# Optimization experiments

Hardware: AMD Instinct MI355X
Metric: run time of the kernel (lower is better)

The kernel has to match this reference:

```python
import jax, jax.numpy as jnp
import numpy as np

C_IN, C_OUT, KH, KW = 64, 128, 3, 3
STRIDE, PAD, DIL = 1, 1, 1
EPS = 1e-5


def setup_inputs() -> dict:
    key = jax.random.key(0)
    ks = jax.random.split(key, 7)
    B, H, W = 8, 112, 112
    x = jax.random.normal(ks[0], (B, C_IN, H, W), dtype=jnp.float32)
    # offset conv: produces 2*KH*KW offset channels; small init keeps offsets sane
    w_off = jax.random.normal(ks[1], (2 * KH * KW, C_IN, KH, KW), dtype=jnp.float32) * 0.01
    b_off = jax.random.normal(ks[2], (2 * KH * KW,), dtype=jnp.float32) * 0.01
    # deformable conv weight/bias
    fan_in = C_IN * KH * KW
    w_dcn = jax.random.normal(ks[3], (C_OUT, C_IN, KH, KW), dtype=jnp.float32) / np.sqrt(fan_in)
    b_dcn = jax.random.normal(ks[4], (C_OUT,), dtype=jnp.float32) * 0.01
    gamma = jnp.ones((C_OUT,), dtype=jnp.float32)
    beta = jnp.zeros((C_OUT,), dtype=jnp.float32)
    return {"x": x, "w_off": w_off, "b_off": b_off, "w_dcn": w_dcn,
            "b_dcn": b_dcn, "gamma": gamma, "beta": beta}


def _conv2d(x, w, b):
    y = jax.lax.conv_general_dilated(
        x, w, window_strides=(STRIDE, STRIDE),
        padding=((PAD, PAD), (PAD, PAD)),
        rhs_dilation=(DIL, DIL),
        dimension_numbers=("NCHW", "OIHW", "NCHW"))
    return y + b[None, :, None, None]


def _deform_conv(x, offset, w, b):
    # x: [B,C,H,W]; offset: [B, 2*KH*KW, Ho, Wo] with (dy, dx) pairs per tap
    B, C, H, W = x.shape
    KK = KH * KW
    Ho, Wo = offset.shape[2], offset.shape[3]
    off = offset.reshape(B, KK, 2, Ho, Wo)
    ky = (jnp.arange(KK) // KW).astype(jnp.float32)  # kernel row per tap
    kx = (jnp.arange(KK) % KW).astype(jnp.float32)
    base_y = (jnp.arange(Ho) * STRIDE - PAD).astype(jnp.float32)
    base_x = (jnp.arange(Wo) * STRIDE - PAD).astype(jnp.float32)
    # sampling positions [B, KK, Ho, Wo]
    py = off[:, :, 0] + base_y[None, None, :, None] + (ky * DIL)[None, :, None, None]
    px = off[:, :, 1] + base_x[None, None, None, :] + (kx * DIL)[None, :, None, None]

    y0 = jnp.floor(py)
    x0 = jnp.floor(px)
    wy1 = py - y0  # weight for y0+1
    wx1 = px - x0
    y0i = y0.astype(jnp.int32)
    x0i = x0.astype(jnp.int32)

    x_flat = x.reshape(B, C, H * W)

    def gather_corner(yi, xi, wgt):
        # yi, xi, wgt: [B, KK, Ho, Wo]
        valid = (yi >= 0) & (yi < H) & (xi >= 0) & (xi < W)
        idx = jnp.clip(yi, 0, H - 1) * W + jnp.clip(xi, 0, W - 1)
        idx = idx.reshape(B, -1)  # [B, KK*Ho*Wo]
        vals = jnp.take_along_axis(x_flat, idx[:, None, :], axis=2)  # [B, C, N]
        coef = (wgt * valid.astype(wgt.dtype)).reshape(B, 1, -1)
        return vals * coef

    samp = (gather_corner(y0i,     x0i,     (1 - wy1) * (1 - wx1))
            + gather_corner(y0i,     x0i + 1, (1 - wy1) * wx1)
            + gather_corner(y0i + 1, x0i,     wy1 * (1 - wx1))
            + gather_corner(y0i + 1, x0i + 1, wy1 * wx1))
    samp = samp.reshape(B, C, KK, Ho, Wo)
    out = jnp.einsum("bckhw,ock->bohw", samp, w.reshape(w.shape[0], C, KK))
    return out + b[None, :, None, None]


def reference(x, w_off, b_off, w_dcn, b_dcn, gamma, beta):
    offset = _conv2d(x, w_off, b_off)
    y = _deform_conv(x, offset, w_dcn, b_dcn)
    # BatchNorm2d (training mode: biased batch stats) + ReLU
    mean = jnp.mean(y, axis=(0, 2, 3))
    var = jnp.var(y, axis=(0, 2, 3))
    yhat = (y - mean[None, :, None, None]) * jax.lax.rsqrt(var + EPS)[None, :, None, None]
    y = gamma[None, :, None, None] * yhat + beta[None, :, None, None]
    return jax.nn.relu(y)
```

## Files before the change

kernel.cpp:

```cpp
#include <hip/hip_runtime.h>

#define H    112
#define W    112
#define HW   12544
#define CIN  64
#define COUT 128
#define BATCH 8
#define KK   9
#define OFFC 18
#define EPS  1e-5f
#define TP   32
#define KDIM 576
#define KHALF 288
#define KPAD2 296
#define NB   3136
#define YPAD 36

typedef unsigned short ushort;
typedef unsigned int uint;
typedef _Float16 half2v __attribute__((ext_vector_type(2)));
typedef _Float16 half8  __attribute__((ext_vector_type(8)));
typedef __attribute__((ext_vector_type(4))) float floatx4;

__device__ __forceinline__ half2v u2h(uint u) {
  union { uint u; half2v h; } c; c.u = u; return c.h;
}
__device__ __forceinline__ uint h2u(half2v h) {
  union { uint u; half2v h; } c; c.h = h; return c.u;
}
__device__ __forceinline__ uint pack_h2(float a, float b) {
  half2v h; h[0] = (_Float16)a; h[1] = (_Float16)b; return h2u(h);
}
__device__ __forceinline__ ushort f2h_bits(float v) {
  union { _Float16 h; ushort u; } c; c.h = (_Float16)v; return c.u;
}
__device__ __forceinline__ float h2f_bits(ushort u) {
  union { ushort u; _Float16 h; } c; c.u = u; return (float)c.h;
}

__global__ __launch_bounds__(256) void k_transpose_x(
    const float* __restrict__ x, ushort* __restrict__ xTh) {
  __shared__ float tile[64][65];
  int b = blockIdx.y;
  int p0 = blockIdx.x * 64;
  int tid = threadIdx.x;
  int j = tid & 63, cb = tid >> 6;
#pragma unroll
  for (int i = 0; i < 16; ++i) {
    int ci = cb * 16 + i;
    tile[ci][j] = x[((size_t)(b * CIN + ci)) * HW + p0 + j];
  }
  __syncthreads();
  int px = tid >> 2, ciq = tid & 3;
#pragma unroll
  for (int g = 0; g < 4; ++g) {
    int ci = ciq * 16 + g * 4;
    uint lo = pack_h2(tile[ci + 0][px], tile[ci + 1][px]);
    uint hi = pack_h2(tile[ci + 2][px], tile[ci + 3][px]);
    *(uint2*)&xTh[((size_t)b * HW + p0 + px) * 64 + ci] = make_uint2(lo, hi);
  }
}

__global__ __launch_bounds__(256) void k_prep_w(
    const float* __restrict__ w_off, const float* __restrict__ w_dcn,
    ushort* __restrict__ w_offT, ushort* __restrict__ w_mf) {
  int i = blockIdx.x * 256 + threadIdx.x;
  if (i < 32 * KDIM) {
    int oc = i / KDIM, k = i - oc * KDIM;
    int kk = k >> 6, ci = k & 63;
    float v = (oc < OFFC) ? w_off[(oc * CIN + ci) * KK + kk] : 0.f;
    w_offT[i] = f2h_bits(v);
  } else if (i < 32 * KDIM + COUT * KDIM) {
    int jj = i - 32 * KDIM;
    int co = jj / KDIM, k = jj - co * KDIM;
    int h = k / KHALF, r = k - h * KHALF;
    int kk = r >> 5, cil = r & 31;
    int ci = h * 32 + cil;
    w_mf[jj] = f2h_bits(w_dcn[(co * CIN + ci) * KK + kk]);
  }
}

__global__ __launch_bounds__(256) void k_offset_conv(
    const ushort* __restrict__ xTh, const ushort* __restrict__ w_offT,
    const float* __restrict__ bias, float* __restrict__ out) {
  int b = blockIdx.y;
  int wave = threadIdx.x >> 6, lane = threadIdx.x & 63;
  int row16 = lane & 15, quad = lane >> 4;
  int p = blockIdx.x * 64 + wave * 16 + row16;
  int ho = p / W, wo = p - ho * W;
  const ushort* xb = xTh + (size_t)b * HW * 64;

  half8 Bf[18];
#pragma unroll
  for (int ks = 0; ks < 18; ++ks) {
    int kk = ks >> 1;
    int ci0 = (ks & 1) * 32 + quad * 8;
    int kh = kk / 3, kw = kk - kh * 3;
    int yy = ho + kh - 1, xx = wo + kw - 1;
    bool valid = (yy >= 0) & (yy < H) & (xx >= 0) & (xx < W);
    half8 v = {0, 0, 0, 0, 0, 0, 0, 0};
    if (valid) v = *(const half8*)(xb + ((size_t)(yy * W + xx) << 6) + ci0);
    Bf[ks] = v;
  }
  floatx4 acc0 = {0.f, 0.f, 0.f, 0.f}, acc1 = acc0;
  const ushort* wa0 = w_offT + row16 * KDIM + quad * 8;
  const ushort* wa1 = w_offT + (16 + row16) * KDIM + quad * 8;
#pragma unroll
  for (int ks = 0; ks < 18; ++ks) {
    half8 A0 = *(const half8*)(wa0 + ks * 32);
    half8 A1 = *(const half8*)(wa1 + ks * 32);
    acc0 = __builtin_amdgcn_mfma_f32_16x16x32_f16(A0, Bf[ks], acc0, 0, 0, 0);
    acc1 = __builtin_amdgcn_mfma_f32_16x16x32_f16(A1, Bf[ks], acc1, 0, 0, 0);
  }
  float* ob = out + (size_t)b * OFFC * HW;
#pragma unroll
  for (int reg = 0; reg < 4; ++reg) {
    int oc = quad * 4 + reg;
    ob[(size_t)oc * HW + p] = acc0[reg] + bias[oc];
    int oc1 = 16 + oc;
    if (oc1 < OFFC) ob[(size_t)oc1 * HW + p] = acc1[reg] + bias[oc1];
  }
}

struct SMemA { uint4 s_wh[KK][TP]; int4 s_i[KK][TP]; ushort samp[TP][KPAD2]; };
struct SMemB { ushort yst[COUT][YPAD]; float stat_s[COUT]; float stat_q[COUT]; };
union SMemU { SMemA a; SMemB b; };

__global__ __launch_bounds__(256) void k_deform(
    const ushort* __restrict__ xTh, const float* __restrict__ off,
    const ushort* __restrict__ w_mf, ushort* __restrict__ y,
    float* __restrict__ psT) {
  __shared__ SMemU sm;

  int b = blockIdx.y;
  int p0 = blockIdx.x * TP;
  int bid = blockIdx.y * gridDim.x + blockIdx.x;
  int tid = threadIdx.x;
  const ushort* xb = xTh + (size_t)b * HW * 64;

  for (int it = tid; it < KK * TP; it += 256) {
    int kk = it >> 5;
    int px = it & 31;
    int p = p0 + px;
    int ho = p / W, wo = p - ho * W;
    float dy = off[((size_t)b * OFFC + 2 * kk) * HW + p];
    float dx = off[((size_t)b * OFFC + 2 * kk + 1) * HW + p];
    float py = dy + (float)(ho - 1 + kk / 3);
    float pxx = dx + (float)(wo - 1 + kk % 3);
    float y0f = floorf(py), x0f = floorf(pxx);
    float wy1 = py - y0f, wx1 = pxx - x0f;
    int y0 = (int)y0f, x0 = (int)x0f;
    int y1 = y0 + 1, x1 = x0 + 1;
    float vy0 = (y0 >= 0 && y0 < H) ? 1.f : 0.f;
    float vy1 = (y1 >= 0 && y1 < H) ? 1.f : 0.f;
    float vx0 = (x0 >= 0 && x0 < W) ? 1.f : 0.f;
    float vx1 = (x1 >= 0 && x1 < W) ? 1.f : 0.f;
    int cy0 = min(max(y0, 0), H - 1), cy1 = min(max(y1, 0), H - 1);
    int cx0 = min(max(x0, 0), W - 1), cx1 = min(max(x1, 0), W - 1);
    float w00 = (1.f - wy1) * (1.f - wx1) * vy0 * vx0;
    float w01 = (1.f - wy1) * wx1 * vy0 * vx1;
    float w10 = wy1 * (1.f - wx1) * vy1 * vx0;
    float w11 = wy1 * wx1 * vy1 * vx1;
    sm.a.s_wh[kk][px] = make_uint4(pack_h2(w00, w00), pack_h2(w01, w01),
                                   pack_h2(w10, w10), pack_h2(w11, w11));
    sm.a.s_i[kk][px] = make_int4((cy0 * W + cx0) << 6, (cy0 * W + cx1) << 6,
                                 (cy1 * W + cx0) << 6, (cy1 * W + cx1) << 6);
  }
  __syncthreads();

  int wave = tid >> 6, lane = tid & 63;
  int row16 = lane & 15, quad = lane >> 4;
  int koff = quad * 8;
  int co_base = wave * 32;
  const ushort* wa0 = w_mf + (size_t)(co_base + row16) * KDIM + koff;
  const ushort* wa1 = w_mf + (size_t)(co_base + 16 + row16) * KDIM + koff;

  floatx4 acc00 = {0.f, 0.f, 0.f, 0.f}, acc01 = acc00, acc10 = acc00, acc11 = acc00;

  for (int h = 0; h < 2; ++h) {
#pragma unroll
    for (int r = 0; r < 5; ++r) {
      int it = tid + r * 256;
      if (it < 1152) {
        int px = it / 36;
        int rem = it - px * 36;
        int kk = rem >> 2;
        int cig = rem & 3;
        int cil0 = cig * 8;
        int cio = h * 32 + cil0;
        uint4 wh = sm.a.s_wh[kk][px];
        int4 iv = sm.a.s_i[kk][px];
        half2v w0 = u2h(wh.x), w1 = u2h(wh.y), w2 = u2h(wh.z), w3 = u2h(wh.w);
        uint4 c0 = *(const uint4*)(xb + iv.x + cio);
        uint4 c1 = *(const uint4*)(xb + iv.y + cio);
        uint4 c2 = *(const uint4*)(xb + iv.z + cio);
        uint4 c3 = *(const uint4*)(xb + iv.w + cio);
        uint4 res;
        res.x = h2u(w0 * u2h(c0.x) + w1 * u2h(c1.x) + w2 * u2h(c2.x) + w3 * u2h(c3.x));
        res.y = h2u(w0 * u2h(c0.y) + w1 * u2h(c1.y) + w2 * u2h(c2.y) + w3 * u2h(c3.y));
        res.z = h2u(w0 * u2h(c0.z) + w1 * u2h(c1.z) + w2 * u2h(c2.z) + w3 * u2h(c3.z));
        res.w = h2u(w0 * u2h(c0.w) + w1 * u2h(c1.w) + w2 * u2h(c2.w) + w3 * u2h(c3.w));
        *(uint4*)&sm.a.samp[px][kk * 32 + cil0] = res;
      }
    }
    __syncthreads();

    const ushort* sb0 = &sm.a.samp[row16][koff];
    const ushort* sb1 = &sm.a.samp[16 + row16][koff];
    const ushort* a0 = wa0 + h * KHALF;
    const ushort* a1 = wa1 + h * KHALF;
#pragma unroll
    for (int ks = 0; ks < 9; ++ks) {
      half8 A0 = *(const half8*)(a0 + ks * 32);
      half8 A1 = *(const half8*)(a1 + ks * 32);
      half8 B0 = *(const half8*)(sb0 + ks * 32);
      half8 B1 = *(const half8*)(sb1 + ks * 32);
      acc00 = __builtin_amdgcn_mfma_f32_16x16x32_f16(A0, B0, acc00, 0, 0, 0);
      acc01 = __builtin_amdgcn_mfma_f32_16x16x32_f16(A0, B1, acc01, 0, 0, 0);
      acc10 = __builtin_amdgcn_mfma_f32_16x16x32_f16(A1, B0, acc10, 0, 0, 0);
      acc11 = __builtin_amdgcn_mfma_f32_16x16x32_f16(A1, B1, acc11, 0, 0, 0);
    }
    __syncthreads();
  }

#pragma unroll
  for (int reg = 0; reg < 4; ++reg) {
    int cA = co_base + quad * 4 + reg;
    int cB = cA + 16;
    sm.b.yst[cA][row16]      = f2h_bits(acc00[reg]);
    sm.b.yst[cA][16 + row16] = f2h_bits(acc01[reg]);
    sm.b.yst[cB][row16]      = f2h_bits(acc10[reg]);
    sm.b.yst[cB][16 + row16] = f2h_bits(acc11[reg]);
    float s0 = acc00[reg] + acc01[reg];
    float q0 = acc00[reg] * acc00[reg] + acc01[reg] * acc01[reg];
    float s1 = acc10[reg] + acc11[reg];
    float q1 = acc10[reg] * acc10[reg] + acc11[reg] * acc11[reg];
#pragma unroll
    for (int m = 1; m < 16; m <<= 1) {
      s0 += __shfl_xor(s0, m, 64);
      q0 += __shfl_xor(q0, m, 64);
      s1 += __shfl_xor(s1, m, 64);
      q1 += __shfl_xor(q1, m, 64);
    }
    if (row16 == 0) {
      sm.b.stat_s[cA] = s0;
      sm.b.stat_q[cA] = q0;
      sm.b.stat_s[cB] = s1;
      sm.b.stat_q[cB] = q1;
    }
  }
  __syncthreads();

  {
    int co = tid >> 1, seg = tid & 1;
    const ushort* row = &sm.b.yst[co][seg * 16];
    uint2 v0 = *(const uint2*)(row + 0);
    uint2 v1 = *(const uint2*)(row + 4);
    uint2 v2 = *(const uint2*)(row + 8);
    uint2 v3 = *(const uint2*)(row + 12);
    ushort* dst = y + (size_t)b * COUT * HW + (size_t)co * HW + p0 + seg * 16;
    *(uint4*)dst       = make_uint4(v0.x, v0.y, v1.x, v1.y);
    *(uint4*)(dst + 8) = make_uint4(v2.x, v2.y, v3.x, v3.y);
    float sv = (tid < 128) ? sm.b.stat_s[tid] : sm.b.stat_q[tid - 128];
    psT[(size_t)bid * 256 + tid] = sv;
  }
}

__global__ __launch_bounds__(256) void k_reduce(const float* __restrict__ psT,
                                                float* __restrict__ stats) {
  int tid = threadIdx.x;
  float s = 0.f;
  for (int i = blockIdx.x; i < NB; i += gridDim.x)
    s += psT[(size_t)i * 256 + tid];
  atomicAdd(&stats[tid], s);
}

__global__ __launch_bounds__(256) void k_norm(const ushort* __restrict__ y,
                                              const float* __restrict__ stats,
                                              const float* __restrict__ gamma,
                                              const float* __restrict__ beta,
                                              float* __restrict__ out) {
  int i8 = blockIdx.x * 256 + threadIdx.x;
  const int total8 = BATCH * COUT * HW / 8;
  if (i8 >= total8) return;
  size_t i = (size_t)i8 * 8;
  int c = (int)((i / HW) & (COUT - 1));
  const float N = (float)(BATCH * HW);
  float m = stats[c] / N;
  float var = stats[COUT + c] / N - m * m;
  float r = rsqrtf(var + EPS);
  float g = gamma[c], bt = beta[c];
  float a = r * g;
  float base = bt - m * a;
  uint4 u = *(const uint4*)&y[i];
  float4 o0, o1;
  half2v h0 = u2h(u.x), h1 = u2h(u.y), h2 = u2h(u.z), h3 = u2h(u.w);
  o0.x = fmaxf(0.f, fmaf((float)h0[0], a, base));
  o0.y = fmaxf(0.f, fmaf((float)h0[1], a, base));
  o0.z = fmaxf(0.f, fmaf((float)h1[0], a, base));
  o0.w = fmaxf(0.f, fmaf((float)h1[1], a, base));
  o1.x = fmaxf(0.f, fmaf((float)h2[0], a, base));
  o1.y = fmaxf(0.f, fmaf((float)h2[1], a, base));
  o1.z = fmaxf(0.f, fmaf((float)h3[0], a, base));
  o1.w = fmaxf(0.f, fmaf((float)h3[1], a, base));
  *(float4*)&out[i]     = o0;
  *(float4*)&out[i + 4] = o1;
}

extern "C" void kernel_launch(void* const* d_in, const int* in_sizes, int n_in,
                              void* d_out, int out_size, void* d_ws, size_t ws_size,
                              hipStream_t stream) {
  const float* x     = (const float*)d_in[0];
  const float* w_off = (const float*)d_in[1];
  const float* b_off = (const float*)d_in[2];
  const float* w_dcn = (const float*)d_in[3];
  const float* gamma = (const float*)d_in[5];
  const float* beta  = (const float*)d_in[6];
  float* out = (float*)d_out;

  float* ws = (float*)d_ws;
  float*  off_buf = ws;
  float*  psT     = off_buf + 1806336;
  float*  stats   = psT + 802816;
  ushort* xTh     = (ushort*)(stats + 256);
  ushort* w_mf    = xTh + 6422528;
  ushort* w_offT  = w_mf + 73728;
  ushort* y_h     = w_offT + 18432;

  hipMemsetAsync(stats, 0, 256 * sizeof(float), stream);
  k_transpose_x<<<dim3(HW / 64, BATCH), 256, 0, stream>>>(x, xTh);
  k_prep_w<<<(32 * KDIM + COUT * KDIM + 255) / 256, 256, 0, stream>>>(w_off, w_dcn, w_offT, w_mf);
  k_offset_conv<<<dim3(HW / 64, BATCH), 256, 0, stream>>>(xTh, w_offT, b_off, off_buf);
  k_deform<<<dim3(HW / TP, BATCH), 256, 0, stream>>>(xTh, off_buf, w_mf, y_h, psT);
  k_reduce<<<64, 256, 0, stream>>>(psT, stats);
  k_norm<<<(BATCH * COUT * HW / 8 + 255) / 256, 256, 0, stream>>>(y_h, stats, gamma, beta, out);
}
```

Measured before the change: 243.0 us.

## Fuse offset conv into deform kernel, merge prep kernels, rewrite stats reduction

The offset convolution is now computed inside the deformable kernel per 32-pixel tile with MFMA and kept in shared memory, which removes the global offset buffer round trip and one launch. The x transpose and weight prep kernels are merged into one launch. The stats reduction now has each block own four channels and reduce over all partial blocks with shuffles, which drops the memset and the atomics. The cost is extra register pressure and latency at the start of the deform kernel.

```diff
diff --git a/kernel.cpp b/kernel.cpp
--- a/kernel.cpp
+++ b/kernel.cpp
@@ -34,91 +34,47 @@
 __device__ __forceinline__ ushort f2h_bits(float v) {
   union { _Float16 h; ushort u; } c; c.h = (_Float16)v; return c.u;
 }
-__device__ __forceinline__ float h2f_bits(ushort u) {
-  union { ushort u; _Float16 h; } c; c.u = u; return (float)c.h;
-}
-
-__global__ __launch_bounds__(256) void k_transpose_x(
-    const float* __restrict__ x, ushort* __restrict__ xTh) {
+
+__global__ __launch_bounds__(256) void k_transpose_prep(
+    const float* __restrict__ x, const float* __restrict__ w_off,
+    const float* __restrict__ w_dcn, ushort* __restrict__ xTh,
+    ushort* __restrict__ w_offT, ushort* __restrict__ w_mf) {
   __shared__ float tile[64][65];
-  int b = blockIdx.y;
-  int p0 = blockIdx.x * 64;
+  int tb = blockIdx.x;
   int tid = threadIdx.x;
-  int j = tid & 63, cb = tid >> 6;
-#pragma unroll
-  for (int i = 0; i < 16; ++i) {
-    int ci = cb * 16 + i;
-    tile[ci][j] = x[((size_t)(b * CIN + ci)) * HW + p0 + j];
-  }
-  __syncthreads();
-  int px = tid >> 2, ciq = tid & 3;
-#pragma unroll
-  for (int g = 0; g < 4; ++g) {
-    int ci = ciq * 16 + g * 4;
-    uint lo = pack_h2(tile[ci + 0][px], tile[ci + 1][px]);
-    uint hi = pack_h2(tile[ci + 2][px], tile[ci + 3][px]);
-    *(uint2*)&xTh[((size_t)b * HW + p0 + px) * 64 + ci] = make_uint2(lo, hi);
-  }
-}
-
-__global__ __launch_bounds__(256) void k_prep_w(
-    const float* __restrict__ w_off, const float* __restrict__ w_dcn,
-    ushort* __restrict__ w_offT, ushort* __restrict__ w_mf) {
-  int i = blockIdx.x * 256 + threadIdx.x;
-  if (i < 32 * KDIM) {
-    int oc = i / KDIM, k = i - oc * KDIM;
-    int kk = k >> 6, ci = k & 63;
-    float v = (oc < OFFC) ? w_off[(oc * CIN + ci) * KK + kk] : 0.f;
-    w_offT[i] = f2h_bits(v);
-  } else if (i < 32 * KDIM + COUT * KDIM) {
-    int jj = i - 32 * KDIM;
-    int co = jj / KDIM, k = jj - co * KDIM;
-    int h = k / KHALF, r = k - h * KHALF;
-    int kk = r >> 5, cil = r & 31;
-    int ci = h * 32 + cil;
-    w_mf[jj] = f2h_bits(w_dcn[(co * CIN + ci) * KK + kk]);
-  }
-}
-
-__global__ __launch_bounds__(256) void k_offset_conv(
-    const ushort* __restrict__ xTh, const ushort* __restrict__ w_offT,
-    const float* __restrict__ bias, float* __restrict__ out) {
-  int b = blockIdx.y;
-  int wave = threadIdx.x >> 6, lane = threadIdx.x & 63;
-  int row16 = lane & 15, quad = lane >> 4;
-  int p = blockIdx.x * 64 + wave * 16 + row16;
-  int ho = p / W, wo = p - ho * W;
-  const ushort* xb = xTh + (size_t)b * HW * 64;
-
-  half8 Bf[18];
-#pragma unroll
-  for (int ks = 0; ks < 18; ++ks) {
-    int kk = ks >> 1;
-    int ci0 = (ks & 1) * 32 + quad * 8;
-    int kh = kk / 3, kw = kk - kh * 3;
-    int yy = ho + kh - 1, xx = wo + kw - 1;
-    bool valid = (yy >= 0) & (yy < H) & (xx >= 0) & (xx < W);
-    half8 v = {0, 0, 0, 0, 0, 0, 0, 0};
-    if (valid) v = *(const half8*)(xb + ((size_t)(yy * W + xx) << 6) + ci0);
-    Bf[ks] = v;
-  }
-  floatx4 acc0 = {0.f, 0.f, 0.f, 0.f}, acc1 = acc0;
-  const ushort* wa0 = w_offT + row16 * KDIM + quad * 8;
-  const ushort* wa1 = w_offT + (16 + row16) * KDIM + quad * 8;
-#pragma unroll
-  for (int ks = 0; ks < 18; ++ks) {
-    half8 A0 = *(const half8*)(wa0 + ks * 32);
-    half8 A1 = *(const half8*)(wa1 + ks * 32);
-    acc0 = __builtin_amdgcn_mfma_f32_16x16x32_f16(A0, Bf[ks], acc0, 0, 0, 0);
-    acc1 = __builtin_amdgcn_mfma_f32_16x16x32_f16(A1, Bf[ks], acc1, 0, 0, 0);
-  }
-  float* ob = out + (size_t)b * OFFC * HW;
-#pragma unroll
-  for (int reg = 0; reg < 4; ++reg) {
-    int oc = quad * 4 + reg;
-    ob[(size_t)oc * HW + p] = acc0[reg] + bias[oc];
-    int oc1 = 16 + oc;
-    if (oc1 < OFFC) ob[(size_t)oc1 * HW + p] = acc1[reg] + bias[oc1];
+  if (tb < 1568) {
+    int b = tb / 196;
+    int p0 = (tb - b * 196) * 64;
+    int j = tid & 63, cb = tid >> 6;
+#pragma unroll
+    for (int i = 0; i < 16; ++i) {
+      int ci = cb * 16 + i;
+      tile[ci][j] = x[((size_t)(b * CIN + ci)) * HW + p0 + j];
+    }
+    __syncthreads();
+    int px = tid >> 2, ciq = tid & 3;
+#pragma unroll
+    for (int g = 0; g < 4; ++g) {
+      int ci = ciq * 16 + g * 4;
+      uint lo = pack_h2(tile[ci + 0][px], tile[ci + 1][px]);
+      uint hi = pack_h2(tile[ci + 2][px], tile[ci + 3][px]);
+      *(uint2*)&xTh[((size_t)b * HW + p0 + px) * 64 + ci] = make_uint2(lo, hi);
+    }
+  } else {
+    int i = (tb - 1568) * 256 + tid;
+    if (i < 32 * KDIM) {
+      int oc = i / KDIM, k = i - oc * KDIM;
+      int kk = k >> 6, ci = k & 63;
+      float v = (oc < OFFC) ? w_off[(oc * CIN + ci) * KK + kk] : 0.f;
+      w_offT[i] = f2h_bits(v);
+    } else if (i < 32 * KDIM + COUT * KDIM) {
+      int jj = i - 32 * KDIM;
+      int co = jj / KDIM, k = jj - co * KDIM;
+      int h = k / KHALF, r = k - h * KHALF;
+      int kk = r >> 5, cil = r & 31;
+      int ci = h * 32 + cil;
+      w_mf[jj] = f2h_bits(w_dcn[(co * CIN + ci) * KK + kk]);
+    }
   }
 }
 
@@ -127,10 +83,11 @@
 union SMemU { SMemA a; SMemB b; };
 
 __global__ __launch_bounds__(256) void k_deform(
-    const ushort* __restrict__ xTh, const float* __restrict__ off,
-    const ushort* __restrict__ w_mf, ushort* __restrict__ y,
-    float* __restrict__ psT) {
+    const ushort* __restrict__ xTh, const ushort* __restrict__ w_offT,
+    const float* __restrict__ b_off, const ushort* __restrict__ w_mf,
+    ushort* __restrict__ y, float* __restrict__ psT) {
   __shared__ SMemU sm;
+  __shared__ float off_s[OFFC][33];
 
   int b = blockIdx.y;
   int p0 = blockIdx.x * TP;
@@ -138,13 +95,53 @@
   int tid = threadIdx.x;
   const ushort* xb = xTh + (size_t)b * HW * 64;
 
+  int wave = tid >> 6, lane = tid & 63;
+  int row16 = lane & 15, quad = lane >> 4;
+
+  {
+    int pxh = wave >> 1, mt = wave & 1;
+    int p = p0 + pxh * 16 + row16;
+    int ho = p / W, wo = p - ho * W;
+    floatx4 oacc = {0.f, 0.f, 0.f, 0.f};
+    const ushort* wa = w_offT + (size_t)(mt * 16 + row16) * KDIM + quad * 8;
+    half8 Bf[9];
+#pragma unroll
+    for (int c = 0; c < 2; ++c) {
+#pragma unroll
+      for (int j = 0; j < 9; ++j) {
+        int ks = c * 9 + j;
+        int kk = ks >> 1;
+        int ci0 = (ks & 1) * 32 + quad * 8;
+        int kh = kk / 3, kw = kk - kh * 3;
+        int yy = ho + kh - 1, xx = wo + kw - 1;
+        bool valid = (yy >= 0) & (yy < H) & (xx >= 0) & (xx < W);
+        half8 v = {0, 0, 0, 0, 0, 0, 0, 0};
+        if (valid) v = *(const half8*)(xb + ((size_t)(yy * W + xx) << 6) + ci0);
+        Bf[j] = v;
+      }
+#pragma unroll
+      for (int j = 0; j < 9; ++j) {
+        int ks = c * 9 + j;
+        half8 A = *(const half8*)(wa + ks * 32);
+        oacc = __builtin_amdgcn_mfma_f32_16x16x32_f16(A, Bf[j], oacc, 0, 0, 0);
+      }
+    }
+#pragma unroll
+    for (int reg = 0; reg < 4; ++reg) {
+      int oc = mt * 16 + quad * 4 + reg;
+      if (oc < OFFC)
+        off_s[oc][pxh * 16 + row16] = oacc[reg] + b_off[oc];
+    }
+  }
+  __syncthreads();
+
   for (int it = tid; it < KK * TP; it += 256) {
     int kk = it >> 5;
     int px = it & 31;
     int p = p0 + px;
     int ho = p / W, wo = p - ho * W;
-    float dy = off[((size_t)b * OFFC + 2 * kk) * HW + p];
-    float dx = off[((size_t)b * OFFC + 2 * kk + 1) * HW + p];
+    float dy = off_s[2 * kk][px];
+    float dx = off_s[2 * kk + 1][px];
     float py = dy + (float)(ho - 1 + kk / 3);
     float pxx = dx + (float)(wo - 1 + kk % 3);
     float y0f = floorf(py), x0f = floorf(pxx);
@@ -168,8 +165,6 @@
   }
   __syncthreads();
 
-  int wave = tid >> 6, lane = tid & 63;
-  int row16 = lane & 15, quad = lane >> 4;
   int koff = quad * 8;
   int co_base = wave * 32;
   const ushort* wa0 = w_mf + (size_t)(co_base + row16) * KDIM + koff;
@@ -268,11 +263,32 @@
 
 __global__ __launch_bounds__(256) void k_reduce(const float* __restrict__ psT,
                                                 float* __restrict__ stats) {
+  int g = blockIdx.x;
   int tid = threadIdx.x;
-  float s = 0.f;
-  for (int i = blockIdx.x; i < NB; i += gridDim.x)
-    s += psT[(size_t)i * 256 + tid];
-  atomicAdd(&stats[tid], s);
+  float4 a = make_float4(0.f, 0.f, 0.f, 0.f);
+  for (int i = tid; i < NB; i += 256) {
+    float4 v = *(const float4*)&psT[(size_t)i * 256 + g * 4];
+    a.x += v.x; a.y += v.y; a.z += v.z; a.w += v.w;
+  }
+#pragma unroll
+  for (int o = 32; o > 0; o >>= 1) {
+    a.x += __shfl_down(a.x, o, 64);
+    a.y += __shfl_down(a.y, o, 64);
+    a.z += __shfl_down(a.z, o, 64);
+    a.w += __shfl_down(a.w, o, 64);
+  }
+  __shared__ float4 ls[4];
+  int lane = tid & 63, wid = tid >> 6;
+  if (lane == 0) ls[wid] = a;
+  __syncthreads();
+  if (tid == 0) {
+    float4 s;
+    s.x = ls[0].x + ls[1].x + ls[2].x + ls[3].x;
+    s.y = ls[0].y + ls[1].y + ls[2].y + ls[3].y;
+    s.z = ls[0].z + ls[1].z + ls[2].z + ls[3].z;
+    s.w = ls[0].w + ls[1].w + ls[2].w + ls[3].w;
+    *(float4*)&stats[g * 4] = s;
+  }
 }
 
 __global__ __launch_bounds__(256) void k_norm(const ushort* __restrict__ y,
@@ -319,19 +335,15 @@
   float* out = (float*)d_out;
 
   float* ws = (float*)d_ws;
-  float*  off_buf = ws;
-  float*  psT     = off_buf + 1806336;
+  float*  psT     = ws;
   float*  stats   = psT + 802816;
   ushort* xTh     = (ushort*)(stats + 256);
   ushort* w_mf    = xTh + 6422528;
   ushort* w_offT  = w_mf + 73728;
   ushort* y_h     = w_offT + 18432;
 
-  hipMemsetAsync(stats, 0, 256 * sizeof(float), stream);
-  k_transpose_x<<<dim3(HW / 64, BATCH), 256, 0, stream>>>(x, xTh);
-  k_prep_w<<<(32 * KDIM + COUT * KDIM + 255) / 256, 256, 0, stream>>>(w_off, w_dcn, w_offT, w_mf);
-  k_offset_conv<<<dim3(HW / 64, BATCH), 256, 0, stream>>>(xTh, w_offT, b_off, off_buf);
-  k_deform<<<dim3(HW / TP, BATCH), 256, 0, stream>>>(xTh, off_buf, w_mf, y_h, psT);
+  k_transpose_prep<<<1928, 256, 0, stream>>>(x, w_off, w_dcn, xTh, w_offT, w_mf);
+  k_deform<<<dim3(HW / TP, BATCH), 256, 0, stream>>>(xTh, w_offT, b_off, w_mf, y_h, psT);
   k_reduce<<<64, 256, 0, stream>>>(psT, stats);
   k_norm<<<(BATCH * COUT * HW / 8 + 255) / 256, 256, 0, stream>>>(y_h, stats, gamma, beta, out);
 }
```

Measured after the change: 237.1 us. 2.4% less time.
